# Kernel tuning notes

Hardware: AMD Instinct MI355X
Metric: run time of the kernel (lower is better)

The kernel has to match this reference:

```python
import jax, jax.numpy as jnp
import numpy as np

B, LVS, WIDTH, DEPTH = 8192, 512, 512, 7
EPS = 1e-5
SLOPE = 0.01  # torch LeakyReLU default negative_slope


def setup_inputs() -> dict:
    key = jax.random.key(0)
    ks = jax.random.split(key, 16)
    inp = {"x": jax.random.normal(ks[0], (B, LVS), dtype=jnp.float32)}
    for i in range(DEPTH):
        fan_in = LVS + WIDTH * i
        inp[f"W{i}"] = jax.random.normal(ks[1 + i], (WIDTH, fan_in), dtype=jnp.float32) / np.sqrt(fan_in)
    inp["b"] = 0.01 * jax.random.normal(ks[8], (DEPTH, WIDTH), dtype=jnp.float32)
    inp["gamma"] = jnp.ones((DEPTH, WIDTH), dtype=jnp.float32)
    inp["beta"] = jnp.zeros((DEPTH, WIDTH), dtype=jnp.float32)
    cin = LVS + DEPTH * WIDTH  # 4096
    inp["Wc"] = jax.random.normal(ks[9], (1, cin), dtype=jnp.float32) / np.sqrt(cin)
    inp["bc"] = jnp.zeros((1,), dtype=jnp.float32)
    # torch: rv = randn(...) * 0.02 + 1, multiplied onto each projection
    inp["noise"] = 1.0 + 0.02 * jax.random.normal(ks[10], (DEPTH, B, WIDTH), dtype=jnp.float32)
    return inp


def reference(x, W0, W1, W2, W3, W4, W5, W6, b, gamma, beta, Wc, bc, noise):
    Ws = (W0, W1, W2, W3, W4, W5, W6)
    last = x
    for i in range(DEPTH):
        # Linear: [B, in_i] @ [in_i, width]
        h = jnp.einsum('bi,wi->bw', last, Ws[i]) + b[i]
        # BatchNorm1d (training mode: batch stats, biased variance)
        mean = jnp.mean(h, axis=0)
        var = jnp.mean(jnp.square(h - mean), axis=0)
        h = (h - mean) * jax.lax.rsqrt(var + EPS) * gamma[i] + beta[i]
        # LeakyReLU + multiplicative noise, fused elementwise
        h = jnp.where(h >= 0, h, SLOPE * h) * noise[i]
        last = jnp.concatenate((last, h), axis=-1)
    logits = jnp.einsum('bi,oi->bo', last, Wc) + bc
    return jax.nn.sigmoid(logits)
```

## Files before the change

kernel.cpp:

```cpp
#include <hip/hip_runtime.h>

#define B_ROWS 8192
#define WIDTH  512
#define DEPTH  7
#define CIN    4096
#define EPS    1e-5f
#define SLOPE  0.01f

typedef __attribute__((ext_vector_type(8))) short short8;
typedef __attribute__((ext_vector_type(4))) short short4v;
typedef __attribute__((ext_vector_type(4))) float f32x4;
typedef __attribute__((ext_vector_type(16))) float f32x16;

__device__ inline short f2bf(float f) {
  unsigned u = __builtin_bit_cast(unsigned, f);
  unsigned r = (u + 0x7FFFu + ((u >> 16) & 1u)) >> 16;
  return (short)r;
}

__device__ inline void gl_lds16(const void* g, void* l) {
  __builtin_amdgcn_global_load_lds(
      (const __attribute__((address_space(1))) unsigned*)g,
      (__attribute__((address_space(3))) unsigned*)l, 16, 0, 0);
}

struct WP { const float* p[7]; };

__global__ __launch_bounds__(256) void convw(WP wp, short* __restrict__ out) {
  long e = ((long)blockIdx.x * 256 + threadIdx.x) * 4;
  int layer; long base;
  if      (e < 262144L)  { layer = 0; base = 0; }
  else if (e < 786432L)  { layer = 1; base = 262144L; }
  else if (e < 1572864L) { layer = 2; base = 786432L; }
  else if (e < 2621440L) { layer = 3; base = 1572864L; }
  else if (e < 3932160L) { layer = 4; base = 2621440L; }
  else if (e < 5505024L) { layer = 5; base = 3932160L; }
  else                   { layer = 6; base = 5505024L; }
  f32x4 v = *(const f32x4*)(wp.p[layer] + (e - base));
  short4v o;
  o.x = f2bf(v.x); o.y = f2bf(v.y); o.z = f2bf(v.z); o.w = f2bf(v.w);
  *(short4v*)(out + e) = o;
}

__global__ __launch_bounds__(256) void initx(const float* __restrict__ x,
                                             const float* __restrict__ wc,
                                             short* __restrict__ lastbf,
                                             float* __restrict__ logit,
                                             float* __restrict__ sumsz) {
  int gid = blockIdx.x * 256 + threadIdx.x;
  if (gid < DEPTH * 1024) sumsz[gid] = 0.f;
  int w = threadIdx.x >> 6, l = threadIdx.x & 63;
  int r = blockIdx.x * 4 + w;
  const float* xr = x + (long)r * 512 + l * 8;
  f32x4 v0 = *(const f32x4*)xr;
  f32x4 v1 = *(const f32x4*)(xr + 4);
  const float* wcr = wc + l * 8;
  float acc = 0.f;
  short8 ob;
#pragma unroll
  for (int j = 0; j < 4; ++j) { acc += v0[j] * wcr[j];     ob[j]     = f2bf(v0[j]); }
#pragma unroll
  for (int j = 0; j < 4; ++j) { acc += v1[j] * wcr[4 + j]; ob[4 + j] = f2bf(v1[j]); }
  *(short8*)&lastbf[(long)r * CIN + l * 8] = ob;
#pragma unroll
  for (int off = 32; off; off >>= 1) acc += __shfl_xor(acc, off);
  if (l == 0) logit[r] = acc;
}

__global__ __launch_bounds__(256, 2) void gemm_fused(const short* __restrict__ A,
                                                     const short* __restrict__ Bw,
                                                     float* __restrict__ C,
                                                     float* __restrict__ sums,
                                                     int K) {
  __shared__ __align__(16) char smem[49152];
  int t = threadIdx.x;
  int ks = t >> 6, l = t & 63;
  int l31 = l & 31, hi = l >> 5;
  int bm = blockIdx.x, bn = blockIdx.y;
  const short* Ab = A + (long)(bm * 128) * CIN;
  const short* Bb = Bw + (long)(bn * 64) * K;

  f32x16 acc[4][2];
#pragma unroll
  for (int m = 0; m < 4; ++m)
#pragma unroll
    for (int n = 0; n < 2; ++n)
#pragma unroll
      for (int r = 0; r < 16; ++r) acc[m][n][r] = 0.f;

  int l8 = l >> 3;
  int scol = ((l & 7) ^ l8) << 3;

#define STAGE(buf, k0)                                                                       \
  {                                                                                          \
    char* base = smem + (buf) * 24576;                                                       \
    int c0 = ks * 4, c1 = ks * 2;                                                            \
    gl_lds16(Ab + (long)((c0    ) * 8 + l8) * CIN + (k0) + scol, base + (c0    ) * 1024);    \
    gl_lds16(Ab + (long)((c0 + 1) * 8 + l8) * CIN + (k0) + scol, base + (c0 + 1) * 1024);    \
    gl_lds16(Ab + (long)((c0 + 2) * 8 + l8) * CIN + (k0) + scol, base + (c0 + 2) * 1024);    \
    gl_lds16(Ab + (long)((c0 + 3) * 8 + l8) * CIN + (k0) + scol, base + (c0 + 3) * 1024);    \
    gl_lds16(Bb + (long)((c1    ) * 8 + l8) * K + (k0) + scol, base + 16384 + (c1    ) * 1024); \
    gl_lds16(Bb + (long)((c1 + 1) * 8 + l8) * K + (k0) + scol, base + 16384 + (c1 + 1) * 1024); \
  }

  STAGE(0, 0);
  __syncthreads();

  int kb = ks * 32 + hi * 16;
  int sw = (l & 7) << 4;

  int nt = K >> 6;
  int cur = 0;
  for (int tix = 0; tix < nt; ++tix) {
    if (tix + 1 < nt) STAGE(cur ^ 1, (tix + 1) << 6);
    const char* AsC = smem + cur * 24576;
    const char* BsC = AsC + 16384;
    short8 a[4], b[2];
#pragma unroll
    for (int m = 0; m < 4; ++m)
      a[m] = *(const short8*)(AsC + (m * 32 + l31) * 128 + (kb ^ sw));
#pragma unroll
    for (int n = 0; n < 2; ++n)
      b[n] = *(const short8*)(BsC + (n * 32 + l31) * 128 + (kb ^ sw));
#pragma unroll
    for (int m = 0; m < 4; ++m)
#pragma unroll
      for (int n = 0; n < 2; ++n)
        acc[m][n] = __builtin_amdgcn_mfma_f32_32x32x16_bf16(a[m], b[n], acc[m][n], 0, 0, 0);
    __syncthreads();
    cur ^= 1;
  }

  float* Red = (float*)smem;
#define RIDX(m, n, r) (((m) * 32 + ((r) & 3) + 8 * ((r) >> 2) + 4 * hi) * 64 + (n) * 32 + l31)
  if (ks == 3) {
#pragma unroll
    for (int m = 0; m < 4; ++m)
#pragma unroll
      for (int n = 0; n < 2; ++n)
#pragma unroll
        for (int r = 0; r < 16; ++r) Red[RIDX(m, n, r)] = acc[m][n][r];
  }
  __syncthreads();
  if (ks == 2) {
#pragma unroll
    for (int m = 0; m < 4; ++m)
#pragma unroll
      for (int n = 0; n < 2; ++n)
#pragma unroll
        for (int r = 0; r < 16; ++r) Red[RIDX(m, n, r)] += acc[m][n][r];
  }
  __syncthreads();
  if (ks == 1) {
#pragma unroll
    for (int m = 0; m < 4; ++m)
#pragma unroll
      for (int n = 0; n < 2; ++n)
#pragma unroll
        for (int r = 0; r < 16; ++r) Red[RIDX(m, n, r)] += acc[m][n][r];
  }
  __syncthreads();
  if (ks == 0) {
    float* Cb = C + (long)(bm * 128) * WIDTH + bn * 64;
#pragma unroll
    for (int n = 0; n < 2; ++n) {
      float s = 0.f, q = 0.f;
#pragma unroll
      for (int m = 0; m < 4; ++m) {
#pragma unroll
        for (int r = 0; r < 16; ++r) {
          int cr = (r & 3) + 8 * (r >> 2) + 4 * hi;
          float v = acc[m][n][r] + Red[RIDX(m, n, r)];
          Cb[(long)(m * 32 + cr) * WIDTH + n * 32 + l31] = v;
          s += v; q += v * v;
        }
      }
      s += __shfl_xor(s, 32);
      q += __shfl_xor(q, 32);
      if (l < 32) {
        int colg = bn * 64 + n * 32 + l;
        atomicAdd(&sums[colg], s);
        atomicAdd(&sums[WIDTH + colg], q);
      }
    }
  }
#undef RIDX
#undef STAGE
}

__global__ __launch_bounds__(256) void bnact(const float* __restrict__ h,
                                             const float* __restrict__ sums,
                                             const float* __restrict__ gamma,
                                             const float* __restrict__ beta,
                                             const float* __restrict__ noise,
                                             const float* __restrict__ wc,
                                             short* __restrict__ lastseg,
                                             float* __restrict__ logit) {
  int w = threadIdx.x >> 6, l = threadIdx.x & 63;
  int r = blockIdx.x * 4 + w;
  int c = l * 8;
  const float invB = 1.0f / 8192.0f;
  f32x4 h0 = *(const f32x4*)&h[(long)r * WIDTH + c];
  f32x4 h1 = *(const f32x4*)&h[(long)r * WIDTH + c + 4];
  f32x4 n0 = *(const f32x4*)&noise[(long)r * WIDTH + c];
  f32x4 n1 = *(const f32x4*)&noise[(long)r * WIDTH + c + 4];
  float acc = 0.f;
  short8 ob;
#pragma unroll
  for (int j = 0; j < 8; ++j) {
    int cc = c + j;
    float hv = j < 4 ? h0[j] : h1[j - 4];
    float nv = j < 4 ? n0[j] : n1[j - 4];
    float mean = sums[cc] * invB;
    float var = sums[WIDTH + cc] * invB - mean * mean;
    float v = (hv - mean) * rsqrtf(var + EPS);
    v = v * gamma[cc] + beta[cc];
    v = v >= 0.f ? v : SLOPE * v;
    v *= nv;
    acc += v * wc[cc];
    ob[j] = f2bf(v);
  }
  *(short8*)&lastseg[(long)r * CIN + c] = ob;
#pragma unroll
  for (int off = 32; off; off >>= 1) acc += __shfl_xor(acc, off);
  if (l == 0) logit[r] += acc;
}

__global__ __launch_bounds__(256) void finalize(const float* __restrict__ logit,
                                                const float* __restrict__ bc,
                                                float* __restrict__ out) {
  int i = blockIdx.x * 256 + threadIdx.x;
  float z = logit[i] + bc[0];
  out[i] = 1.0f / (1.0f + expf(-z));
}

extern "C" void kernel_launch(void* const* d_in, const int* in_sizes, int n_in,
                              void* d_out, int out_size, void* d_ws, size_t ws_size,
                              hipStream_t stream) {
  (void)in_sizes; (void)n_in; (void)out_size; (void)ws_size;
  const float* x     = (const float*)d_in[0];
  WP wp;
  for (int i = 0; i < 7; ++i) wp.p[i] = (const float*)d_in[1 + i];
  const float* gamma = (const float*)d_in[9];
  const float* beta  = (const float*)d_in[10];
  const float* Wc    = (const float*)d_in[11];
  const float* bc    = (const float*)d_in[12];
  const float* noise = (const float*)d_in[13];

  char* ws = (char*)d_ws;
  short* lastbf = (short*)ws;
  float* hpre   = (float*)(ws + 67108864);
  short* wbf    = (short*)(ws + 67108864 + 16777216);
  float* sums   = (float*)(ws + 67108864 + 16777216 + 14680064);
  float* logit  = (float*)(ws + 67108864 + 16777216 + 14680064 + 28672);

  convw<<<7168, 256, 0, stream>>>(wp, wbf);
  initx<<<2048, 256, 0, stream>>>(x, Wc, lastbf, logit, sums);

  long woff = 0;
  for (int i = 0; i < DEPTH; ++i) {
    int K = 512 * (i + 1);
    gemm_fused<<<dim3(64, 8), 256, 0, stream>>>(lastbf, wbf + woff, hpre,
                                                sums + i * 1024, K);
    bnact<<<2048, 256, 0, stream>>>(hpre, sums + i * 1024,
                                    gamma + i * 512, beta + i * 512,
                                    noise + (long)i * B_ROWS * WIDTH,
                                    Wc + 512 + i * 512,
                                    lastbf + 512 + (long)i * 512, logit);
    woff += (long)512 * K;
  }
  finalize<<<32, 256, 0, stream>>>(logit, bc, (float*)d_out);
}
```

Measured before the change: 287.9 us.

## Store pre-BN activations as bf16, merge prolog kernels, raise GEMM occupancy hint

The GEMM epilogue now writes pre-normalization activations as bf16 instead of fp32, which halves the intermediate write and the re-read in the BN/activation kernel. Batch statistics are still accumulated from the fp32 values. The weight conversion and input initialization kernels are merged into one launch. The GEMM launch bound goes from 2 to 3 blocks per SM, which may force register spills. Normalizing from bf16-rounded values adds a small precision loss.

```diff
diff --git a/kernel.cpp b/kernel.cpp
--- a/kernel.cpp
+++ b/kernel.cpp
@@ -18,6 +18,11 @@
   return (short)r;
 }
 
+__device__ inline float bf2f(short b) {
+  unsigned u = ((unsigned)(unsigned short)b) << 16;
+  return __builtin_bit_cast(float, u);
+}
+
 __device__ inline void gl_lds16(const void* g, void* l) {
   __builtin_amdgcn_global_load_lds(
       (const __attribute__((address_space(1))) unsigned*)g,
@@ -26,27 +31,28 @@
 
 struct WP { const float* p[7]; };
 
-__global__ __launch_bounds__(256) void convw(WP wp, short* __restrict__ out) {
-  long e = ((long)blockIdx.x * 256 + threadIdx.x) * 4;
-  int layer; long base;
-  if      (e < 262144L)  { layer = 0; base = 0; }
-  else if (e < 786432L)  { layer = 1; base = 262144L; }
-  else if (e < 1572864L) { layer = 2; base = 786432L; }
-  else if (e < 2621440L) { layer = 3; base = 1572864L; }
-  else if (e < 3932160L) { layer = 4; base = 2621440L; }
-  else if (e < 5505024L) { layer = 5; base = 3932160L; }
-  else                   { layer = 6; base = 5505024L; }
-  f32x4 v = *(const f32x4*)(wp.p[layer] + (e - base));
-  short4v o;
-  o.x = f2bf(v.x); o.y = f2bf(v.y); o.z = f2bf(v.z); o.w = f2bf(v.w);
-  *(short4v*)(out + e) = o;
-}
-
-__global__ __launch_bounds__(256) void initx(const float* __restrict__ x,
-                                             const float* __restrict__ wc,
-                                             short* __restrict__ lastbf,
-                                             float* __restrict__ logit,
-                                             float* __restrict__ sumsz) {
+__global__ __launch_bounds__(256) void prolog(WP wp, short* __restrict__ wbf,
+                                              const float* __restrict__ x,
+                                              const float* __restrict__ wc,
+                                              short* __restrict__ lastbf,
+                                              float* __restrict__ logit,
+                                              float* __restrict__ sumsz) {
+  if (blockIdx.x >= 2048) {
+    long e = ((long)(blockIdx.x - 2048) * 256 + threadIdx.x) * 4;
+    int layer; long base;
+    if      (e < 262144L)  { layer = 0; base = 0; }
+    else if (e < 786432L)  { layer = 1; base = 262144L; }
+    else if (e < 1572864L) { layer = 2; base = 786432L; }
+    else if (e < 2621440L) { layer = 3; base = 1572864L; }
+    else if (e < 3932160L) { layer = 4; base = 2621440L; }
+    else if (e < 5505024L) { layer = 5; base = 3932160L; }
+    else                   { layer = 6; base = 5505024L; }
+    f32x4 v = *(const f32x4*)(wp.p[layer] + (e - base));
+    short4v o;
+    o.x = f2bf(v.x); o.y = f2bf(v.y); o.z = f2bf(v.z); o.w = f2bf(v.w);
+    *(short4v*)(wbf + e) = o;
+    return;
+  }
   int gid = blockIdx.x * 256 + threadIdx.x;
   if (gid < DEPTH * 1024) sumsz[gid] = 0.f;
   int w = threadIdx.x >> 6, l = threadIdx.x & 63;
@@ -67,9 +73,9 @@
   if (l == 0) logit[r] = acc;
 }
 
-__global__ __launch_bounds__(256, 2) void gemm_fused(const short* __restrict__ A,
+__global__ __launch_bounds__(256, 3) void gemm_fused(const short* __restrict__ A,
                                                      const short* __restrict__ Bw,
-                                                     float* __restrict__ C,
+                                                     short* __restrict__ C,
                                                      float* __restrict__ sums,
                                                      int K) {
   __shared__ __align__(16) char smem[49152];
@@ -161,7 +167,7 @@
   }
   __syncthreads();
   if (ks == 0) {
-    float* Cb = C + (long)(bm * 128) * WIDTH + bn * 64;
+    short* Cb = C + (long)(bm * 128) * WIDTH + bn * 64;
 #pragma unroll
     for (int n = 0; n < 2; ++n) {
       float s = 0.f, q = 0.f;
@@ -171,7 +177,7 @@
         for (int r = 0; r < 16; ++r) {
           int cr = (r & 3) + 8 * (r >> 2) + 4 * hi;
           float v = acc[m][n][r] + Red[RIDX(m, n, r)];
-          Cb[(long)(m * 32 + cr) * WIDTH + n * 32 + l31] = v;
+          Cb[(long)(m * 32 + cr) * WIDTH + n * 32 + l31] = f2bf(v);
           s += v; q += v * v;
         }
       }
@@ -188,7 +194,7 @@
 #undef STAGE
 }
 
-__global__ __launch_bounds__(256) void bnact(const float* __restrict__ h,
+__global__ __launch_bounds__(256) void bnact(const short* __restrict__ h,
                                              const float* __restrict__ sums,
                                              const float* __restrict__ gamma,
                                              const float* __restrict__ beta,
@@ -200,8 +206,7 @@
   int r = blockIdx.x * 4 + w;
   int c = l * 8;
   const float invB = 1.0f / 8192.0f;
-  f32x4 h0 = *(const f32x4*)&h[(long)r * WIDTH + c];
-  f32x4 h1 = *(const f32x4*)&h[(long)r * WIDTH + c + 4];
+  short8 hb = *(const short8*)&h[(long)r * WIDTH + c];
   f32x4 n0 = *(const f32x4*)&noise[(long)r * WIDTH + c];
   f32x4 n1 = *(const f32x4*)&noise[(long)r * WIDTH + c + 4];
   float acc = 0.f;
@@ -209,7 +214,7 @@
 #pragma unroll
   for (int j = 0; j < 8; ++j) {
     int cc = c + j;
-    float hv = j < 4 ? h0[j] : h1[j - 4];
+    float hv = bf2f(hb[j]);
     float nv = j < 4 ? n0[j] : n1[j - 4];
     float mean = sums[cc] * invB;
     float var = sums[WIDTH + cc] * invB - mean * mean;
@@ -249,13 +254,12 @@
 
   char* ws = (char*)d_ws;
   short* lastbf = (short*)ws;
-  float* hpre   = (float*)(ws + 67108864);
+  short* hpre   = (short*)(ws + 67108864);
   short* wbf    = (short*)(ws + 67108864 + 16777216);
   float* sums   = (float*)(ws + 67108864 + 16777216 + 14680064);
   float* logit  = (float*)(ws + 67108864 + 16777216 + 14680064 + 28672);
 
-  convw<<<7168, 256, 0, stream>>>(wp, wbf);
-  initx<<<2048, 256, 0, stream>>>(x, Wc, lastbf, logit, sums);
+  prolog<<<9216, 256, 0, stream>>>(wp, wbf, x, Wc, lastbf, logit, sums);
 
   long woff = 0;
   for (int i = 0; i < DEPTH; ++i) {
```

Result: slower. 331.7 us (+15.2%).
